# Performance work log

Hardware: AMD Instinct MI355X
Metric: run time of the kernel (lower is better)

## Reference

```python
import jax, jax.numpy as jnp
import numpy as np

HEADS = 4
DIM_HEAD = 32
SCALE = DIM_HEAD ** -0.5


def setup_inputs() -> dict:
    key = jax.random.key(0)
    k1, k2, k3 = jax.random.split(key, 3)
    dim = 256
    hidden = HEADS * DIM_HEAD  # 128
    x = jax.random.normal(k1, (2, dim, 64, 64), dtype=jnp.float32)
    # Conv2d 1x1 weights flattened to [out_ch, in_ch]
    w_qkv = jax.random.normal(k2, (hidden * 3, dim), dtype=jnp.float32) * (dim ** -0.5)
    w_out = jax.random.normal(k3, (dim, hidden), dtype=jnp.float32) * (hidden ** -0.5)
    b_out = jnp.zeros((dim,), dtype=jnp.float32)
    return {"x": x, "w_qkv": w_qkv, "w_out": w_out, "b_out": b_out}


def reference(x, w_qkv, w_out, b_out):
    b, c, h, w = x.shape
    n = h * w
    # 1x1 conv == channel matmul: [b, 3*hidden, h, w]
    qkv = jnp.einsum('bchw,oc->bohw', x, w_qkv)
    q, k, v = jnp.split(qkv, 3, axis=1)
    # 'b (heads d) x y -> b heads d (x y)'
    def to_heads(t):
        return t.reshape(b, HEADS, DIM_HEAD, n)
    q, k, v = to_heads(q), to_heads(k), to_heads(v)
    q = q * SCALE
    dots = jnp.einsum('bhdi,bhdj->bhij', q, k)  # [b, heads, n, n]
    dots = dots - jax.lax.stop_gradient(jnp.max(dots, axis=-1, keepdims=True))
    attn = jax.nn.softmax(dots, axis=-1)
    out = jnp.einsum('bhij,bhdj->bhid', attn, v)  # [b, heads, n, d]
    # 'b heads (x y) d -> b (heads d) x y'
    out = out.transpose(0, 1, 3, 2).reshape(b, HEADS * DIM_HEAD, h, w)
    return jnp.einsum('bchw,oc->bohw', out, w_out) + b_out[None, :, None, None]
```

## Files before the change

### kernel.cpp

```cpp
#include <hip/hip_runtime.h>
#include <hip/hip_bf16.h>
#include <math.h>

#define NB 2
#define CIN 256
#define NPOS 4096
#define HID 128
#define NHEAD 4
#define DHEAD 32
#define NBH 8
#define NSPLIT 4
#define QSCALE 0.2550348676144781f

typedef __bf16 bf16;
typedef __attribute__((ext_vector_type(8))) __bf16 bf16x8;
typedef __attribute__((ext_vector_type(4))) __bf16 bf16x4;
typedef __attribute__((ext_vector_type(4))) float f32x4;

union B8 { bf16x8 v; bf16x4 h[2]; };

#define XT_OFF  0u
#define QB_OFF  4194304u
#define KB_OFF  6291456u
#define VT_OFF  8388608u
#define AOP_OFF 10485760u
#define LP_OFF  18874368u
#define WB_OFF  19398656u
#define WOB_OFF 19595264u

__global__ __launch_bounds__(256) void prep_kernel(const float* __restrict__ x,
                                                   const float* __restrict__ wqkv,
                                                   const float* __restrict__ wout,
                                                   bf16* __restrict__ xt,
                                                   bf16* __restrict__ wb,
                                                   bf16* __restrict__ wob) {
    const int t = threadIdx.x;
    if (blockIdx.y == 4) {
        int tid = blockIdx.x * 256 + t;
        if (blockIdx.z == 0) {
            #pragma unroll
            for (int u = 0; u < 6; ++u) {
                int idx = tid * 6 + u;
                float v = wqkv[idx];
                if (idx < 32768) v *= QSCALE;
                wb[idx] = (bf16)v;
            }
        } else {
            wob[tid * 2]     = (bf16)wout[tid * 2];
            wob[tid * 2 + 1] = (bf16)wout[tid * 2 + 1];
        }
        return;
    }
    const int b  = blockIdx.z;
    const int c0 = blockIdx.y * 64;
    const int i0 = blockIdx.x * 64;
    __shared__ float Ts[64][65];
    const float* xb = x + (size_t)b * CIN * NPOS;
    #pragma unroll
    for (int u = 0; u < 4; ++u) {
        int c = (t >> 4) + u * 16;
        int i = (t & 15) * 4;
        float4 v = *(const float4*)(xb + (size_t)(c0 + c) * NPOS + i0 + i);
        Ts[c][i] = v.x; Ts[c][i + 1] = v.y; Ts[c][i + 2] = v.z; Ts[c][i + 3] = v.w;
    }
    __syncthreads();
    int i  = t & 63;
    int cc = (t >> 6) * 16;
    B8 o0, o1;
    #pragma unroll
    for (int j = 0; j < 8; ++j) {
        o0.v[j] = (bf16)Ts[cc + j][i];
        o1.v[j] = (bf16)Ts[cc + 8 + j][i];
    }
    bf16* dst = xt + ((size_t)b * NPOS + i0 + i) * CIN + c0 + cc;
    *(bf16x8*)dst       = o0.v;
    *(bf16x8*)(dst + 8) = o1.v;
}

__global__ __launch_bounds__(256) void qkv_kernel(const bf16* __restrict__ xt,
                                                  const bf16* __restrict__ wb,
                                                  bf16* __restrict__ qb,
                                                  bf16* __restrict__ kb,
                                                  bf16* __restrict__ vtb) {
    const int i0 = blockIdx.x * 64;
    const int ot = blockIdx.y * 64;
    const int b  = blockIdx.z;
    const int t  = threadIdx.x;
    const int w  = t >> 6;
    const int lane = t & 63;
    const int quad = lane >> 4;
    const int li   = lane & 15;

    __shared__ bf16 Bs[64][36];

    f32x4 acc[4];
    #pragma unroll
    for (int n = 0; n < 4; ++n) acc[n] = (f32x4){0.f, 0.f, 0.f, 0.f};

    const bf16* xrow = xt + ((size_t)b * NPOS + i0) * CIN;
    const int si = t >> 2;
    const int sk = (t & 3) * 8;

    for (int k0 = 0; k0 < CIN; k0 += 32) {
        __syncthreads();
        B8 g0;
        g0.v = *(const bf16x8*)(xrow + (size_t)si * CIN + k0 + sk);
        *(bf16x4*)&Bs[si][sk]     = g0.h[0];
        *(bf16x4*)&Bs[si][sk + 4] = g0.h[1];
        __syncthreads();
        bf16x8 afrag = *(const bf16x8*)(wb + (size_t)(ot + w * 16 + li) * CIN + k0 + quad * 8);
        #pragma unroll
        for (int n = 0; n < 4; ++n) {
            B8 bf;
            bf.h[0] = *(const bf16x4*)&Bs[n * 16 + li][quad * 8];
            bf.h[1] = *(const bf16x4*)&Bs[n * 16 + li][quad * 8 + 4];
            acc[n] = __builtin_amdgcn_mfma_f32_16x16x32_bf16(afrag, bf.v, acc[n], 0, 0, 0);
        }
    }

    const int obase = ot + w * 16;
    const int sect  = obase >> 7;
    const int oo    = obase & 127;
    const int h     = oo >> 5;
    const int dbase = (oo & 31) + quad * 4;
    const int bh    = b * NHEAD + h;

    #pragma unroll
    for (int n = 0; n < 4; ++n) {
        int i = i0 + n * 16 + li;
        f32x4 v = acc[n];
        if (sect <= 1) {
            bf16x4 pk;
            #pragma unroll
            for (int r = 0; r < 4; ++r) pk[r] = (bf16)v[r];
            bf16* base = (sect == 0) ? qb : kb;
            *(bf16x4*)(base + ((size_t)bh * NPOS + i) * DHEAD + dbase) = pk;
        } else {
            #pragma unroll
            for (int r = 0; r < 4; ++r)
                vtb[((size_t)bh * DHEAD + dbase + r) * NPOS + i] = (bf16)v[r];
        }
    }
}

__global__ __launch_bounds__(256, 4) void fattn_kernel(const bf16* __restrict__ qb,
                                                       const bf16* __restrict__ kb,
                                                       const bf16* __restrict__ vtb,
                                                       bf16* __restrict__ aop,
                                                       float* __restrict__ lpart) {
    const int id    = blockIdx.x;
    const int g     = id & 31;
    const int iblk  = id >> 5;
    const int bh    = g >> 2;
    const int split = g & 3;
    const int w     = threadIdx.x >> 6;
    const int lane  = threadIdx.x & 63;
    const int quad  = lane >> 4;
    const int li    = lane & 15;
    const int i0    = iblk * 128 + w * 32;
    const int j_lo  = split * 1024;

    const bf16* qrow = qb + (size_t)bh * NPOS * DHEAD;
    const bf16x8 qf0 = *(const bf16x8*)(qrow + (size_t)(i0 + li) * DHEAD + quad * 8);
    const bf16x8 qf1 = *(const bf16x8*)(qrow + (size_t)(i0 + 16 + li) * DHEAD + quad * 8);
    const bf16* kbase  = kb  + (size_t)bh * NPOS * DHEAD;
    const bf16* vtbase = vtb + (size_t)bh * DHEAD * NPOS;

    bf16x8 ones;
    #pragma unroll
    for (int j = 0; j < 8; ++j) ones[j] = (bf16)1.0f;

    f32x4 o00 = {0.f,0.f,0.f,0.f}, o01 = {0.f,0.f,0.f,0.f};
    f32x4 o10 = {0.f,0.f,0.f,0.f}, o11 = {0.f,0.f,0.f,0.f};
    f32x4 l0  = {0.f,0.f,0.f,0.f}, l1  = {0.f,0.f,0.f,0.f};

    __shared__ alignas(16) bf16 Kbuf[2][64][32];
    __shared__ alignas(16) bf16 Vbuf[2][32][64];
    __shared__ alignas(16) bf16 plds[4][32][68];

    const f32x4 zero = {0.f,0.f,0.f,0.f};

    const int krow = w * 16 + (lane >> 2);
    const int kcol = (lane & 3) * 8;
    const int vrow = w * 8 + (lane >> 3);
    const int vchk = lane & 7;
    const int vslot = vchk ^ (vrow & 7);
    const bf16* ksrc = kbase + (size_t)krow * DHEAD + kcol;
    const bf16* vsrc = vtbase + (size_t)vrow * NPOS + vchk * 8;

    bf16x8 kg, vg;

    kg = *(const bf16x8*)(ksrc + (size_t)j_lo * DHEAD);
    vg = *(const bf16x8*)(vsrc + j_lo);
    *(bf16x8*)&Kbuf[0][krow][kcol]      = kg;
    *(bf16x8*)&Vbuf[0][vrow][vslot * 8] = vg;
    __syncthreads();

    for (int it = 0; it < 16; ++it) {
        const int cur = it & 1;
        const int j0  = j_lo + it * 64;
        if (it < 15) {
            kg = *(const bf16x8*)(ksrc + (size_t)(j0 + 64) * DHEAD);
            vg = *(const bf16x8*)(vsrc + j0 + 64);
        }
        bf16x8 kf[4];
        #pragma unroll
        for (int tt = 0; tt < 4; ++tt)
            kf[tt] = *(const bf16x8*)&Kbuf[cur][16 * tt + li][quad * 8];
        f32x4 s0[4], s1[4];
        #pragma unroll
        for (int tt = 0; tt < 4; ++tt) {
            s0[tt] = __builtin_amdgcn_mfma_f32_16x16x32_bf16(kf[tt], qf0, zero, 0, 0, 0);
            s1[tt] = __builtin_amdgcn_mfma_f32_16x16x32_bf16(kf[tt], qf1, zero, 0, 0, 0);
        }
        #pragma unroll
        for (int tt = 0; tt < 4; ++tt) {
            bf16x4 p0, p1;
            #pragma unroll
            for (int r = 0; r < 4; ++r) {
                p0[r] = (bf16)__builtin_amdgcn_exp2f(s0[tt][r]);
                p1[r] = (bf16)__builtin_amdgcn_exp2f(s1[tt][r]);
            }
            *(bf16x4*)&plds[w][li][16 * tt + quad * 4]      = p0;
            *(bf16x4*)&plds[w][16 + li][16 * tt + quad * 4] = p1;
        }
        #pragma unroll
        for (int h2 = 0; h2 < 2; ++h2) {
            B8 pf0, pf1;
            pf0.h[0] = *(const bf16x4*)&plds[w][li][h2 * 32 + quad * 8];
            pf0.h[1] = *(const bf16x4*)&plds[w][li][h2 * 32 + quad * 8 + 4];
            pf1.h[0] = *(const bf16x4*)&plds[w][16 + li][h2 * 32 + quad * 8];
            pf1.h[1] = *(const bf16x4*)&plds[w][16 + li][h2 * 32 + quad * 8 + 4];
            const int s0s = (h2 * 4 + quad) ^ (li & 7);
            bf16x8 v0f = *(const bf16x8*)&Vbuf[cur][li][s0s * 8];
            bf16x8 v1f = *(const bf16x8*)&Vbuf[cur][16 + li][s0s * 8];
            l0  = __builtin_amdgcn_mfma_f32_16x16x32_bf16(ones, pf0.v, l0,  0, 0, 0);
            l1  = __builtin_amdgcn_mfma_f32_16x16x32_bf16(ones, pf1.v, l1,  0, 0, 0);
            o00 = __builtin_amdgcn_mfma_f32_16x16x32_bf16(v0f,  pf0.v, o00, 0, 0, 0);
            o01 = __builtin_amdgcn_mfma_f32_16x16x32_bf16(v1f,  pf0.v, o01, 0, 0, 0);
            o10 = __builtin_amdgcn_mfma_f32_16x16x32_bf16(v0f,  pf1.v, o10, 0, 0, 0);
            o11 = __builtin_amdgcn_mfma_f32_16x16x32_bf16(v1f,  pf1.v, o11, 0, 0, 0);
        }
        if (it < 15) {
            *(bf16x8*)&Kbuf[cur ^ 1][krow][kcol]      = kg;
            *(bf16x8*)&Vbuf[cur ^ 1][vrow][vslot * 8] = vg;
        }
        __syncthreads();
    }

    const int b = bh >> 2, h = bh & 3;
    {
        const int i = i0 + li;
        bf16* dst = aop + (((size_t)(split * NB + b) * NPOS + i) * HID) + h * DHEAD;
        bf16x4 pk0, pk1;
        #pragma unroll
        for (int r = 0; r < 4; ++r) { pk0[r] = (bf16)o00[r]; pk1[r] = (bf16)o01[r]; }
        *(bf16x4*)(dst + quad * 4)      = pk0;
        *(bf16x4*)(dst + 16 + quad * 4) = pk1;
        if (quad == 0) lpart[((size_t)split * NBH + bh) * NPOS + i] = l0[0];
    }
    {
        const int i = i0 + 16 + li;
        bf16* dst = aop + (((size_t)(split * NB + b) * NPOS + i) * HID) + h * DHEAD;
        bf16x4 pk0, pk1;
        #pragma unroll
        for (int r = 0; r < 4; ++r) { pk0[r] = (bf16)o10[r]; pk1[r] = (bf16)o11[r]; }
        *(bf16x4*)(dst + quad * 4)      = pk0;
        *(bf16x4*)(dst + 16 + quad * 4) = pk1;
        if (quad == 0) lpart[((size_t)split * NBH + bh) * NPOS + i] = l1[0];
    }
}

__global__ __launch_bounds__(256) void proj_kernel(const bf16* __restrict__ aop,
                                                   const float* __restrict__ lpart,
                                                   const bf16* __restrict__ wob,
                                                   const float* __restrict__ bout,
                                                   float* __restrict__ y) {
    const int i0 = blockIdx.x * 64;
    const int ot = blockIdx.y * 64;
    const int b  = blockIdx.z;
    const int t  = threadIdx.x;
    const int w  = t >> 6;
    const int lane = t & 63;
    const int quad = lane >> 4;
    const int li   = lane & 15;

    __shared__ bf16 Bs[64][132];

    {
        const int row = t >> 2;
        const int cp  = (t & 3) * 32;
        const int gi  = i0 + row;
        const int h   = cp >> 5;

        float lsum = 0.f;
        #pragma unroll
        for (int s = 0; s < NSPLIT; ++s)
            lsum += lpart[((size_t)s * NBH + b * NHEAD + h) * NPOS + gi];
        const float invl = __builtin_amdgcn_rcpf(lsum);

        float vals[32];
        #pragma unroll
        for (int j = 0; j < 32; ++j) vals[j] = 0.f;
        #pragma unroll
        for (int s = 0; s < NSPLIT; ++s) {
            const bf16* src = aop + (((size_t)(s * NB + b) * NPOS + gi) * HID) + cp;
            #pragma unroll
            for (int m = 0; m < 4; ++m) {
                bf16x8 u = *(const bf16x8*)(src + m * 8);
                #pragma unroll
                for (int j = 0; j < 8; ++j) vals[m * 8 + j] += (float)u[j];
            }
        }
        #pragma unroll
        for (int m = 0; m < 4; ++m) {
            B8 pk;
            #pragma unroll
            for (int j = 0; j < 8; ++j) pk.v[j] = (bf16)(vals[m * 8 + j] * invl);
            *(bf16x8*)&Bs[row][cp + m * 8] = pk.v;
        }
    }
    __syncthreads();

    f32x4 acc[4];
    #pragma unroll
    for (int n = 0; n < 4; ++n) acc[n] = (f32x4){0.f, 0.f, 0.f, 0.f};

    #pragma unroll
    for (int k0 = 0; k0 < HID; k0 += 32) {
        bf16x8 afrag = *(const bf16x8*)(wob + (size_t)(ot + w * 16 + li) * HID + k0 + quad * 8);
        #pragma unroll
        for (int n = 0; n < 4; ++n) {
            B8 bf;
            bf.h[0] = *(const bf16x4*)&Bs[n * 16 + li][k0 + quad * 8];
            bf.h[1] = *(const bf16x4*)&Bs[n * 16 + li][k0 + quad * 8 + 4];
            acc[n] = __builtin_amdgcn_mfma_f32_16x16x32_bf16(afrag, bf.v, acc[n], 0, 0, 0);
        }
    }

    float bias[4];
    #pragma unroll
    for (int r = 0; r < 4; ++r) bias[r] = bout[ot + w * 16 + quad * 4 + r];
    float* yb = y + (size_t)b * CIN * NPOS;
    #pragma unroll
    for (int n = 0; n < 4; ++n) {
        int i = i0 + n * 16 + li;
        #pragma unroll
        for (int r = 0; r < 4; ++r)
            yb[(size_t)(ot + w * 16 + quad * 4 + r) * NPOS + i] = acc[n][r] + bias[r];
    }
}

extern "C" void kernel_launch(void* const* d_in, const int* in_sizes, int n_in,
                              void* d_out, int out_size, void* d_ws, size_t ws_size,
                              hipStream_t stream) {
    const float* x    = (const float*)d_in[0];
    const float* wqkv = (const float*)d_in[1];
    const float* wout = (const float*)d_in[2];
    const float* bout = (const float*)d_in[3];
    float* y = (float*)d_out;
    char* ws = (char*)d_ws;

    bf16*  xt  = (bf16*)(ws + XT_OFF);
    bf16*  qb  = (bf16*)(ws + QB_OFF);
    bf16*  kb  = (bf16*)(ws + KB_OFF);
    bf16*  vtb = (bf16*)(ws + VT_OFF);
    bf16*  aop = (bf16*)(ws + AOP_OFF);
    float* lp  = (float*)(ws + LP_OFF);
    bf16*  wb  = (bf16*)(ws + WB_OFF);
    bf16*  wob = (bf16*)(ws + WOB_OFF);

    prep_kernel<<<dim3(64, 5, 2), 256, 0, stream>>>(x, wqkv, wout, xt, wb, wob);
    qkv_kernel<<<dim3(64, 6, 2), 256, 0, stream>>>(xt, wb, qb, kb, vtb);
    fattn_kernel<<<dim3(1024), 256, 0, stream>>>(qb, kb, vtb, aop, lp);
    proj_kernel<<<dim3(64, 4, 2), 256, 0, stream>>>(aop, lp, wob, bout, y);
}
```

Baseline: 110.7 us.

## Retile output projection so each block covers all output channels for 16 positions

The projection kernel now gives each block 16 positions and all 256 output channels, in place of 64 positions by 64 output channels. The split-attention partial sums are therefore read and combined once per position instead of once per output-channel tile, which cuts redundant global reads of the partial outputs. The cost is that each block reloads the full output weight matrix and writes only 16 contiguous floats per output row, which gives narrower store segments.

```diff
diff --git a/kernel.cpp b/kernel.cpp
--- a/kernel.cpp
+++ b/kernel.cpp
@@ -276,20 +276,19 @@
                                                    const bf16* __restrict__ wob,
                                                    const float* __restrict__ bout,
                                                    float* __restrict__ y) {
-    const int i0 = blockIdx.x * 64;
-    const int ot = blockIdx.y * 64;
-    const int b  = blockIdx.z;
+    const int i0 = blockIdx.x * 16;
+    const int b  = blockIdx.y;
     const int t  = threadIdx.x;
     const int w  = t >> 6;
     const int lane = t & 63;
     const int quad = lane >> 4;
     const int li   = lane & 15;
 
-    __shared__ bf16 Bs[64][132];
+    __shared__ bf16 Bs[16][132];
 
     {
-        const int row = t >> 2;
-        const int cp  = (t & 3) * 32;
+        const int row = t >> 4;
+        const int cp  = (t & 15) * 8;
         const int gi  = i0 + row;
         const int h   = cp >> 5;
 
@@ -299,55 +298,46 @@
             lsum += lpart[((size_t)s * NBH + b * NHEAD + h) * NPOS + gi];
         const float invl = __builtin_amdgcn_rcpf(lsum);
 
-        float vals[32];
-        #pragma unroll
-        for (int j = 0; j < 32; ++j) vals[j] = 0.f;
+        float vals[8];
+        #pragma unroll
+        for (int j = 0; j < 8; ++j) vals[j] = 0.f;
         #pragma unroll
         for (int s = 0; s < NSPLIT; ++s) {
-            const bf16* src = aop + (((size_t)(s * NB + b) * NPOS + gi) * HID) + cp;
-            #pragma unroll
-            for (int m = 0; m < 4; ++m) {
-                bf16x8 u = *(const bf16x8*)(src + m * 8);
-                #pragma unroll
-                for (int j = 0; j < 8; ++j) vals[m * 8 + j] += (float)u[j];
-            }
-        }
+            bf16x8 u = *(const bf16x8*)(aop + (((size_t)(s * NB + b) * NPOS + gi) * HID) + cp);
+            #pragma unroll
+            for (int j = 0; j < 8; ++j) vals[j] += (float)u[j];
+        }
+        B8 pk;
+        #pragma unroll
+        for (int j = 0; j < 8; ++j) pk.v[j] = (bf16)(vals[j] * invl);
+        *(bf16x4*)&Bs[row][cp]     = pk.h[0];
+        *(bf16x4*)&Bs[row][cp + 4] = pk.h[1];
+    }
+    __syncthreads();
+
+    f32x4 acc[4];
+    #pragma unroll
+    for (int m = 0; m < 4; ++m) acc[m] = (f32x4){0.f, 0.f, 0.f, 0.f};
+
+    #pragma unroll
+    for (int k0 = 0; k0 < HID; k0 += 32) {
+        B8 bf;
+        bf.h[0] = *(const bf16x4*)&Bs[li][k0 + quad * 8];
+        bf.h[1] = *(const bf16x4*)&Bs[li][k0 + quad * 8 + 4];
         #pragma unroll
         for (int m = 0; m < 4; ++m) {
-            B8 pk;
-            #pragma unroll
-            for (int j = 0; j < 8; ++j) pk.v[j] = (bf16)(vals[m * 8 + j] * invl);
-            *(bf16x8*)&Bs[row][cp + m * 8] = pk.v;
-        }
-    }
-    __syncthreads();
-
-    f32x4 acc[4];
-    #pragma unroll
-    for (int n = 0; n < 4; ++n) acc[n] = (f32x4){0.f, 0.f, 0.f, 0.f};
-
-    #pragma unroll
-    for (int k0 = 0; k0 < HID; k0 += 32) {
-        bf16x8 afrag = *(const bf16x8*)(wob + (size_t)(ot + w * 16 + li) * HID + k0 + quad * 8);
-        #pragma unroll
-        for (int n = 0; n < 4; ++n) {
-            B8 bf;
-            bf.h[0] = *(const bf16x4*)&Bs[n * 16 + li][k0 + quad * 8];
-            bf.h[1] = *(const bf16x4*)&Bs[n * 16 + li][k0 + quad * 8 + 4];
-            acc[n] = __builtin_amdgcn_mfma_f32_16x16x32_bf16(afrag, bf.v, acc[n], 0, 0, 0);
-        }
-    }
-
-    float bias[4];
-    #pragma unroll
-    for (int r = 0; r < 4; ++r) bias[r] = bout[ot + w * 16 + quad * 4 + r];
+            bf16x8 afrag = *(const bf16x8*)(wob + (size_t)(w * 64 + m * 16 + li) * HID + k0 + quad * 8);
+            acc[m] = __builtin_amdgcn_mfma_f32_16x16x32_bf16(afrag, bf.v, acc[m], 0, 0, 0);
+        }
+    }
+
     float* yb = y + (size_t)b * CIN * NPOS;
     #pragma unroll
-    for (int n = 0; n < 4; ++n) {
-        int i = i0 + n * 16 + li;
+    for (int m = 0; m < 4; ++m) {
+        const int oc = w * 64 + m * 16 + quad * 4;
         #pragma unroll
         for (int r = 0; r < 4; ++r)
-            yb[(size_t)(ot + w * 16 + quad * 4 + r) * NPOS + i] = acc[n][r] + bias[r];
+            yb[(size_t)(oc + r) * NPOS + i0 + li] = acc[m][r] + bout[oc + r];
     }
 }
 
@@ -373,5 +363,5 @@
     prep_kernel<<<dim3(64, 5, 2), 256, 0, stream>>>(x, wqkv, wout, xt, wb, wob);
     qkv_kernel<<<dim3(64, 6, 2), 256, 0, stream>>>(xt, wb, qb, kb, vtb);
     fattn_kernel<<<dim3(1024), 256, 0, stream>>>(qb, kb, vtb, aop, lp);
-    proj_kernel<<<dim3(64, 4, 2), 256, 0, stream>>>(aop, lp, wob, bout, y);
-}
+    proj_kernel<<<dim3(256, 2), 256, 0, stream>>>(aop, lp, wob, bout, y);
+}
```

New measurement: 107.9 us. -2.6%, faster.
